# Kernel optimization log

Hardware: AMD Instinct MI355X
Metric: run time of the kernel (lower is better)

## Reference

```python
import jax, jax.numpy as jnp
import numpy as np

N_NODES = 50000
N_EDGES = 800000
IN_FEATS = 64
HIDDEN = 64
NUM_CLASSES = 32


def _graph_conv(x, src, dst, W, b, n_nodes):
    # DGL GraphConv, norm='both', allow_zero_in_degree=True:
    # out = D_in^{-1/2} * (A^T @ (D_out^{-1/2} * x)) @ W + b, degrees clamped to >=1
    e = src.shape[0]
    ones = jnp.ones((e,), dtype=x.dtype)
    out_deg = jax.ops.segment_sum(ones, src, num_segments=n_nodes)
    in_deg = jax.ops.segment_sum(ones, dst, num_segments=n_nodes)
    norm_src = jax.lax.rsqrt(jnp.maximum(out_deg, 1.0))[:, None]
    norm_dst = jax.lax.rsqrt(jnp.maximum(in_deg, 1.0))[:, None]
    h = x * norm_src                                   # [N, d]
    agg = jax.ops.segment_sum(h[src], dst, num_segments=n_nodes)  # gather+scatter over edges
    return (agg * norm_dst) @ W + b


def setup_inputs() -> dict:
    key = jax.random.key(0)
    k1, k2, k3, k4, k5 = jax.random.split(key, 5)
    features = jax.random.normal(k1, (N_NODES, IN_FEATS), dtype=jnp.float32)
    src = jax.random.randint(k2, (N_EDGES,), 0, N_NODES, dtype=jnp.int32)
    dst = jax.random.randint(k3, (N_EDGES,), 0, N_NODES, dtype=jnp.int32)
    W1 = jax.random.normal(k4, (IN_FEATS, HIDDEN), dtype=jnp.float32) * (1.0 / np.sqrt(IN_FEATS))
    b1 = jnp.zeros((HIDDEN,), dtype=jnp.float32)
    W2 = jax.random.normal(k5, (HIDDEN, NUM_CLASSES), dtype=jnp.float32) * (1.0 / np.sqrt(HIDDEN))
    b2 = jnp.zeros((NUM_CLASSES,), dtype=jnp.float32)
    return {"features": features, "src": src, "dst": dst,
            "W1": W1, "b1": b1, "W2": W2, "b2": b2}


def reference(features, src, dst, W1, b1, W2, b2) -> jnp.ndarray:
    n = features.shape[0]
    h = jax.nn.relu(_graph_conv(features, src, dst, W1, b1, n))
    out = _graph_conv(h, src, dst, W2, b2, n)
    # single canonical etype -> mean over one-element stack is identity
    return out
```

## Files before the change

### kernel.cpp

```cpp
#include <hip/hip_runtime.h>
#include <hip/hip_bf16.h>

#define N_NODES 50000
#define N_EDGES 800000
#define F 64
#define C 32
#define CAP 48

#define NPB   800
#define EPB   1000
#define NBUCK 196
#define SEGCAP 5120

#define G1_BLOCKS   2048
#define GOUT_BLOCKS 2048

static __device__ __forceinline__ float bflo(int u) {
    return __uint_as_float(((unsigned)u) << 16);
}
static __device__ __forceinline__ float bfhi(int u) {
    return __uint_as_float(((unsigned)u) & 0xffff0000u);
}
static __device__ __forceinline__ unsigned short f2bf(float f) {
    __hip_bfloat16 h = __float2bfloat16(f);
    return *reinterpret_cast<unsigned short*>(&h);
}

__global__ void part_fused_kernel(const int* __restrict__ src, const int* __restrict__ dst,
                                  int* __restrict__ odeg, int* __restrict__ gseg,
                                  int* __restrict__ edge_d) {
    __shared__ int hd[NBUCK];
    int t = threadIdx.x;
    for (int i = t; i < NBUCK; i += 256) hd[i] = 0;
    __syncthreads();
    int b0 = blockIdx.x * EPB;
    const int4* s4 = reinterpret_cast<const int4*>(src + b0);
    const int4* d4 = reinterpret_cast<const int4*>(dst + b0);
    for (int i = t; i < EPB / 4; i += 256) {
        int4 dv = d4[i];
        int4 sv = s4[i];
        atomicAdd(&hd[dv.x >> 8], 1); atomicAdd(&hd[dv.y >> 8], 1);
        atomicAdd(&hd[dv.z >> 8], 1); atomicAdd(&hd[dv.w >> 8], 1);
        atomicAdd(&odeg[sv.x], 1); atomicAdd(&odeg[sv.y], 1);
        atomicAdd(&odeg[sv.z], 1); atomicAdd(&odeg[sv.w], 1);
    }
    __syncthreads();
    for (int i = t; i < NBUCK; i += 256) {
        int c = hd[i];
        int base = atomicAdd(&gseg[i], c);
        hd[i] = i * SEGCAP + base;
    }
    __syncthreads();
    for (int i = t; i < EPB / 4; i += 256) {
        int4 dv = d4[i];
        int4 sv = s4[i];
        int p;
        p = atomicAdd(&hd[dv.x >> 8], 1); edge_d[p] = ((dv.x & 255) << 16) | sv.x;
        p = atomicAdd(&hd[dv.y >> 8], 1); edge_d[p] = ((dv.y & 255) << 16) | sv.y;
        p = atomicAdd(&hd[dv.z >> 8], 1); edge_d[p] = ((dv.z & 255) << 16) | sv.z;
        p = atomicAdd(&hd[dv.w >> 8], 1); edge_d[p] = ((dv.w & 255) << 16) | sv.w;
    }
}

__global__ void bucket_build_kernel(const int* __restrict__ edge_d,
                                    const int* __restrict__ gseg,
                                    const int* __restrict__ odeg,
                                    unsigned short* __restrict__ csr,
                                    float4* __restrict__ meta) {
    __shared__ int cur[256];
    int t = threadIdx.x;
    int bucket = blockIdx.x;
    cur[t] = 0;
    __syncthreads();
    int len = gseg[bucket];
    if (len > SEGCAP) len = SEGCAP;
    int lo = bucket * SEGCAP, hi = lo + len;
    for (int i = lo + t; i < hi; i += 256) {
        int pd = edge_d[i];
        int dlow = pd >> 16;
        int s = pd & 0xFFFF;
        int pos = atomicAdd(&cur[dlow], 1);
        if (pos < CAP)
            csr[(size_t)(bucket * 256 + dlow) * CAP + pos] = (unsigned short)s;
    }
    __syncthreads();
    int node = bucket * 256 + t;
    if (node < N_NODES) {
        int c = cur[t] < CAP ? cur[t] : CAP;
        float4 m;
        m.x = rsqrtf(fmaxf((float)c, 1.0f));
        m.y = rsqrtf(fmaxf((float)odeg[node], 1.0f));
        m.z = __int_as_float(c);
        m.w = 0.f;
        meta[node] = m;
    }
}

__global__ void gemm_y_kernel(const float* __restrict__ x,
                              const float4* __restrict__ meta,
                              const float* __restrict__ W,
                              __hip_bfloat16* __restrict__ y) {
    __shared__ float sW[F * F];
    __shared__ float srow[16][F];
    int t = threadIdx.x;
    for (int i = t; i < F * F; i += 256) sW[i] = W[i];
    int j = t & 63;
    int w = t >> 6;
    int base = blockIdx.x * 16;
    for (int r = w; r < 16; r += 4) srow[r][j] = x[(size_t)(base + r) * F + j];
    __syncthreads();
    float a0 = 0, a1 = 0, a2 = 0, a3 = 0;
#pragma unroll
    for (int k = 0; k < F; k++) {
        float wv = sW[k * F + j];
        a0 += srow[w * 4 + 0][k] * wv;
        a1 += srow[w * 4 + 1][k] * wv;
        a2 += srow[w * 4 + 2][k] * wv;
        a3 += srow[w * 4 + 3][k] * wv;
    }
    int n0 = base + w * 4;
    y[(size_t)(n0 + 0) * F + j] = __float2bfloat16(a0 * meta[n0 + 0].y);
    y[(size_t)(n0 + 1) * F + j] = __float2bfloat16(a1 * meta[n0 + 1].y);
    y[(size_t)(n0 + 2) * F + j] = __float2bfloat16(a2 * meta[n0 + 2].y);
    y[(size_t)(n0 + 3) * F + j] = __float2bfloat16(a3 * meta[n0 + 3].y);
}

__global__ void gather64_gemv_kernel(const __hip_bfloat16* __restrict__ y,
                                     const unsigned short* __restrict__ csr,
                                     const float4* __restrict__ meta,
                                     const float* __restrict__ b1,
                                     const float* __restrict__ W2,
                                     __hip_bfloat16* __restrict__ gt) {
    __shared__ float sW[F * C];
    int t = threadIdx.x;
    for (int i = t; i < F * C; i += 256) sW[i] = W2[i];
    __syncthreads();
    int w    = t >> 6;
    int lane = t & 63;
    int g  = lane >> 3;
    int fo = (lane & 7) * 8;
    int j    = lane & 31;
    int half = lane >> 5;
    const float4 b1a = *reinterpret_cast<const float4*>(b1 + fo);
    const float4 b1b = *reinterpret_cast<const float4*>(b1 + fo + 4);
    const unsigned short* ytab = reinterpret_cast<const unsigned short*>(y);
    const int STRIDE = G1_BLOCKS * 4;

    int node = blockIdx.x * 4 + w;
    float4 pm = meta[node];
    const unsigned short* prow = csr + (size_t)node * CAP;
    int pr0 = prow[g], pr1 = prow[8 + g], pr2 = prow[16 + g];

    while (node < N_NODES) {
        float nd = pm.x, ns = pm.y;
        int n = __float_as_int(pm.z);
        int r0 = pr0, r1 = pr1, r2 = pr2;
        int nxt = node + STRIDE;
        int pf = (nxt < N_NODES) ? nxt : node;

        int ss0 = (g      < n) ? r0 : 0;  float m0 = (g      < n) ? 1.f : 0.f;
        int ss1 = (8  + g < n) ? r1 : 0;  float m1 = (8  + g < n) ? 1.f : 0.f;
        int ss2 = (16 + g < n) ? r2 : 0;  float m2 = (16 + g < n) ? 1.f : 0.f;

        const int4 v0 = *reinterpret_cast<const int4*>(ytab + (size_t)ss0 * F + fo);
        const int4 v1 = *reinterpret_cast<const int4*>(ytab + (size_t)ss1 * F + fo);
        const int4 v2 = *reinterpret_cast<const int4*>(ytab + (size_t)ss2 * F + fo);

        pm = meta[pf];
        const unsigned short* nrow = csr + (size_t)pf * CAP;
        pr0 = nrow[g]; pr1 = nrow[8 + g]; pr2 = nrow[16 + g];

        float a0, a1, a2, a3, a4, a5, a6, a7;
        a0 = m0 * bflo(v0.x); a1 = m0 * bfhi(v0.x);
        a2 = m0 * bflo(v0.y); a3 = m0 * bfhi(v0.y);
        a4 = m0 * bflo(v0.z); a5 = m0 * bfhi(v0.z);
        a6 = m0 * bflo(v0.w); a7 = m0 * bfhi(v0.w);

#define G1_ACC(vv, mm)                                                        \
        a0 = fmaf(mm, bflo(vv.x), a0); a1 = fmaf(mm, bfhi(vv.x), a1);         \
        a2 = fmaf(mm, bflo(vv.y), a2); a3 = fmaf(mm, bfhi(vv.y), a3);         \
        a4 = fmaf(mm, bflo(vv.z), a4); a5 = fmaf(mm, bfhi(vv.z), a5);         \
        a6 = fmaf(mm, bflo(vv.w), a6); a7 = fmaf(mm, bfhi(vv.w), a7);
        G1_ACC(v1, m1)
        G1_ACC(v2, m2)

        if (__builtin_expect(n > 24, 0)) {
            const unsigned short* row = csr + (size_t)node * CAP;
            int r3 = row[24 + g], r4 = row[32 + g], r5 = row[40 + g];
            int ss3 = (24 + g < n) ? r3 : 0;  float m3 = (24 + g < n) ? 1.f : 0.f;
            int ss4 = (32 + g < n) ? r4 : 0;  float m4 = (32 + g < n) ? 1.f : 0.f;
            int ss5 = (40 + g < n) ? r5 : 0;  float m5 = (40 + g < n) ? 1.f : 0.f;
            const int4 v3 = *reinterpret_cast<const int4*>(ytab + (size_t)ss3 * F + fo);
            const int4 v4 = *reinterpret_cast<const int4*>(ytab + (size_t)ss4 * F + fo);
            const int4 v5 = *reinterpret_cast<const int4*>(ytab + (size_t)ss5 * F + fo);
            G1_ACC(v3, m3)
            G1_ACC(v4, m4)
            G1_ACC(v5, m5)
        }
#undef G1_ACC

#define G1_RED(mk)                                                           \
        a0 += __shfl_xor(a0, mk); a1 += __shfl_xor(a1, mk);                  \
        a2 += __shfl_xor(a2, mk); a3 += __shfl_xor(a3, mk);                  \
        a4 += __shfl_xor(a4, mk); a5 += __shfl_xor(a5, mk);                  \
        a6 += __shfl_xor(a6, mk); a7 += __shfl_xor(a7, mk);
        G1_RED(8)
        G1_RED(16)
        G1_RED(32)
#undef G1_RED

        float hh[8];
        hh[0] = fmaxf(fmaf(a0, nd, b1a.x), 0.f) * ns;
        hh[1] = fmaxf(fmaf(a1, nd, b1a.y), 0.f) * ns;
        hh[2] = fmaxf(fmaf(a2, nd, b1a.z), 0.f) * ns;
        hh[3] = fmaxf(fmaf(a3, nd, b1a.w), 0.f) * ns;
        hh[4] = fmaxf(fmaf(a4, nd, b1b.x), 0.f) * ns;
        hh[5] = fmaxf(fmaf(a5, nd, b1b.y), 0.f) * ns;
        hh[6] = fmaxf(fmaf(a6, nd, b1b.z), 0.f) * ns;
        hh[7] = fmaxf(fmaf(a7, nd, b1b.w), 0.f) * ns;

        float o = 0.f;
#pragma unroll
        for (int k = 0; k < 32; k++) {
            float hv = __shfl(hh[k & 7], (half << 2) + (k >> 3));
            o = fmaf(hv, sW[(half * 32 + k) * C + j], o);
        }
        o += __shfl_down(o, 32);
        if (half == 0)
            __builtin_nontemporal_store(f2bf(o),
                reinterpret_cast<unsigned short*>(gt) + (size_t)node * C + j);
        node = nxt;
    }
}

__global__ void gather_out_kernel(const __hip_bfloat16* __restrict__ gt,
                                  const unsigned short* __restrict__ csr,
                                  const float4* __restrict__ meta,
                                  const float* __restrict__ b2,
                                  float* __restrict__ out) {
    int t = threadIdx.x;
    int w = t >> 6;
    int lane = t & 63;
    int g  = lane >> 3;
    int fo = (lane & 7) * 4;
    const unsigned short* tab = reinterpret_cast<const unsigned short*>(gt);
    const float4 bb = *reinterpret_cast<const float4*>(b2 + fo);
    const int STRIDE = GOUT_BLOCKS * 4;

    int node = blockIdx.x * 4 + w;
    float4 pm = meta[node];
    const unsigned short* prow = csr + (size_t)node * CAP;
    int pr0 = prow[g], pr1 = prow[8 + g], pr2 = prow[16 + g];

    while (node < N_NODES) {
        float nd = pm.x;
        int n = __float_as_int(pm.z);
        int r0 = pr0, r1 = pr1, r2 = pr2;
        int nxt = node + STRIDE;
        int pf = (nxt < N_NODES) ? nxt : node;

        int ss0 = (g      < n) ? r0 : 0;  float m0 = (g      < n) ? 1.f : 0.f;
        int ss1 = (8  + g < n) ? r1 : 0;  float m1 = (8  + g < n) ? 1.f : 0.f;
        int ss2 = (16 + g < n) ? r2 : 0;  float m2 = (16 + g < n) ? 1.f : 0.f;

        const int2 v0 = *reinterpret_cast<const int2*>(tab + (size_t)ss0 * C + fo);
        const int2 v1 = *reinterpret_cast<const int2*>(tab + (size_t)ss1 * C + fo);
        const int2 v2 = *reinterpret_cast<const int2*>(tab + (size_t)ss2 * C + fo);

        pm = meta[pf];
        const unsigned short* nrow = csr + (size_t)pf * CAP;
        pr0 = nrow[g]; pr1 = nrow[8 + g]; pr2 = nrow[16 + g];

        float a0, a1, a2, a3;
        a0 = m0 * bflo(v0.x); a1 = m0 * bfhi(v0.x);
        a2 = m0 * bflo(v0.y); a3 = m0 * bfhi(v0.y);

#define G2_ACC(vv, mm)                                                        \
        a0 = fmaf(mm, bflo(vv.x), a0); a1 = fmaf(mm, bfhi(vv.x), a1);         \
        a2 = fmaf(mm, bflo(vv.y), a2); a3 = fmaf(mm, bfhi(vv.y), a3);
        G2_ACC(v1, m1)
        G2_ACC(v2, m2)

        if (__builtin_expect(n > 24, 0)) {
            const unsigned short* row = csr + (size_t)node * CAP;
            int r3 = row[24 + g], r4 = row[32 + g], r5 = row[40 + g];
            int ss3 = (24 + g < n) ? r3 : 0;  float m3 = (24 + g < n) ? 1.f : 0.f;
            int ss4 = (32 + g < n) ? r4 : 0;  float m4 = (32 + g < n) ? 1.f : 0.f;
            int ss5 = (40 + g < n) ? r5 : 0;  float m5 = (40 + g < n) ? 1.f : 0.f;
            const int2 v3 = *reinterpret_cast<const int2*>(tab + (size_t)ss3 * C + fo);
            const int2 v4 = *reinterpret_cast<const int2*>(tab + (size_t)ss4 * C + fo);
            const int2 v5 = *reinterpret_cast<const int2*>(tab + (size_t)ss5 * C + fo);
            G2_ACC(v3, m3)
            G2_ACC(v4, m4)
            G2_ACC(v5, m5)
        }
#undef G2_ACC

        a0 += __shfl_xor(a0, 8);  a1 += __shfl_xor(a1, 8);
        a2 += __shfl_xor(a2, 8);  a3 += __shfl_xor(a3, 8);
        a0 += __shfl_xor(a0, 16); a1 += __shfl_xor(a1, 16);
        a2 += __shfl_xor(a2, 16); a3 += __shfl_xor(a3, 16);
        a0 += __shfl_xor(a0, 32); a1 += __shfl_xor(a1, 32);
        a2 += __shfl_xor(a2, 32); a3 += __shfl_xor(a3, 32);

        if (lane < 8) {
            float o0 = fmaf(a0, nd, bb.x);
            float o1 = fmaf(a1, nd, bb.y);
            float o2 = fmaf(a2, nd, bb.z);
            float o3 = fmaf(a3, nd, bb.w);
            unsigned long long p0 = ((unsigned long long)__float_as_uint(o0)) |
                                    ((unsigned long long)__float_as_uint(o1) << 32);
            unsigned long long p1 = ((unsigned long long)__float_as_uint(o2)) |
                                    ((unsigned long long)__float_as_uint(o3) << 32);
            unsigned long long* po = reinterpret_cast<unsigned long long*>(
                out + (size_t)node * C + fo);
            __builtin_nontemporal_store(p0, po);
            __builtin_nontemporal_store(p1, po + 1);
        }
        node = nxt;
    }
}

extern "C" void kernel_launch(void* const* d_in, const int* in_sizes, int n_in,
                              void* d_out, int out_size, void* d_ws, size_t ws_size,
                              hipStream_t stream) {
    const float* features = (const float*)d_in[0];
    const int*   src      = (const int*)d_in[1];
    const int*   dst      = (const int*)d_in[2];
    const float* W1       = (const float*)d_in[3];
    const float* b1       = (const float*)d_in[4];
    const float* W2       = (const float*)d_in[5];
    const float* b2       = (const float*)d_in[6];
    float* out = (float*)d_out;

    char* p = (char*)d_ws;
    float4* meta = (float4*)p;            p += (size_t)N_NODES * 16;
    unsigned short* csr = (unsigned short*)p; p += (size_t)N_NODES * CAP * 2;
    __hip_bfloat16* y  = (__hip_bfloat16*)p;  p += (size_t)N_NODES * F * 2;
    __hip_bfloat16* gt = (__hip_bfloat16*)p;

    int* edge_d = (int*)y;
    int* odeg   = (int*)gt;
    int* gseg   = odeg + N_NODES;

    hipMemsetAsync(odeg, 0, (size_t)(N_NODES + 256) * 4, stream);

    part_fused_kernel<<<NPB, 256, 0, stream>>>(src, dst, odeg, gseg, edge_d);
    bucket_build_kernel<<<NBUCK, 256, 0, stream>>>(edge_d, gseg, odeg, csr, meta);

    gemm_y_kernel<<<N_NODES / 16, 256, 0, stream>>>(features, meta, W1, y);
    gather64_gemv_kernel<<<G1_BLOCKS, 256, 0, stream>>>(y, csr, meta, b1, W2, gt);

    gather_out_kernel<<<GOUT_BLOCKS, 256, 0, stream>>>(gt, csr, meta, b2, out);
}
```

Measured before the change: 198.2 us.

## Compute out-degrees via bucketed source partition instead of global atomics

Out-degree counting no longer uses 800k global atomics on an odeg array. Source low bytes are partitioned into per-bucket segments using shared-memory histograms, and each bucket block then counts per-node out-degree in shared memory. This removes the scattered global atomics and shrinks the memset to the segment counters. In exchange it writes and reads an extra byte-per-edge array and adds a second counting pass in the bucket kernel.

```diff
diff --git a/kernel.cpp b/kernel.cpp
--- a/kernel.cpp
+++ b/kernel.cpp
@@ -27,11 +27,11 @@
 }
 
 __global__ void part_fused_kernel(const int* __restrict__ src, const int* __restrict__ dst,
-                                  int* __restrict__ odeg, int* __restrict__ gseg,
-                                  int* __restrict__ edge_d) {
-    __shared__ int hd[NBUCK];
-    int t = threadIdx.x;
-    for (int i = t; i < NBUCK; i += 256) hd[i] = 0;
+                                  int* __restrict__ gseg,
+                                  int* __restrict__ edge_d, unsigned char* __restrict__ edge_s) {
+    __shared__ int hd[NBUCK], hs[NBUCK];
+    int t = threadIdx.x;
+    for (int i = t; i < NBUCK; i += 256) { hd[i] = 0; hs[i] = 0; }
     __syncthreads();
     int b0 = blockIdx.x * EPB;
     const int4* s4 = reinterpret_cast<const int4*>(src + b0);
@@ -41,14 +41,13 @@
         int4 sv = s4[i];
         atomicAdd(&hd[dv.x >> 8], 1); atomicAdd(&hd[dv.y >> 8], 1);
         atomicAdd(&hd[dv.z >> 8], 1); atomicAdd(&hd[dv.w >> 8], 1);
-        atomicAdd(&odeg[sv.x], 1); atomicAdd(&odeg[sv.y], 1);
-        atomicAdd(&odeg[sv.z], 1); atomicAdd(&odeg[sv.w], 1);
+        atomicAdd(&hs[sv.x >> 8], 1); atomicAdd(&hs[sv.y >> 8], 1);
+        atomicAdd(&hs[sv.z >> 8], 1); atomicAdd(&hs[sv.w >> 8], 1);
     }
     __syncthreads();
     for (int i = t; i < NBUCK; i += 256) {
-        int c = hd[i];
-        int base = atomicAdd(&gseg[i], c);
-        hd[i] = i * SEGCAP + base;
+        hd[i] = i * SEGCAP + atomicAdd(&gseg[i], hd[i]);
+        hs[i] = i * SEGCAP + atomicAdd(&gseg[NBUCK + i], hs[i]);
     }
     __syncthreads();
     for (int i = t; i < EPB / 4; i += 256) {
@@ -59,23 +58,29 @@
         p = atomicAdd(&hd[dv.y >> 8], 1); edge_d[p] = ((dv.y & 255) << 16) | sv.y;
         p = atomicAdd(&hd[dv.z >> 8], 1); edge_d[p] = ((dv.z & 255) << 16) | sv.z;
         p = atomicAdd(&hd[dv.w >> 8], 1); edge_d[p] = ((dv.w & 255) << 16) | sv.w;
+        p = atomicAdd(&hs[sv.x >> 8], 1); edge_s[p] = (unsigned char)(sv.x & 255);
+        p = atomicAdd(&hs[sv.y >> 8], 1); edge_s[p] = (unsigned char)(sv.y & 255);
+        p = atomicAdd(&hs[sv.z >> 8], 1); edge_s[p] = (unsigned char)(sv.z & 255);
+        p = atomicAdd(&hs[sv.w >> 8], 1); edge_s[p] = (unsigned char)(sv.w & 255);
     }
 }
 
 __global__ void bucket_build_kernel(const int* __restrict__ edge_d,
+                                    const unsigned char* __restrict__ edge_s,
                                     const int* __restrict__ gseg,
-                                    const int* __restrict__ odeg,
                                     unsigned short* __restrict__ csr,
                                     float4* __restrict__ meta) {
     __shared__ int cur[256];
+    __shared__ int hsm[256];
     int t = threadIdx.x;
     int bucket = blockIdx.x;
     cur[t] = 0;
-    __syncthreads();
-    int len = gseg[bucket];
-    if (len > SEGCAP) len = SEGCAP;
-    int lo = bucket * SEGCAP, hi = lo + len;
-    for (int i = lo + t; i < hi; i += 256) {
+    hsm[t] = 0;
+    __syncthreads();
+    int lend = gseg[bucket];           if (lend > SEGCAP) lend = SEGCAP;
+    int lens = gseg[NBUCK + bucket];   if (lens > SEGCAP) lens = SEGCAP;
+    int lo = bucket * SEGCAP;
+    for (int i = lo + t; i < lo + lend; i += 256) {
         int pd = edge_d[i];
         int dlow = pd >> 16;
         int s = pd & 0xFFFF;
@@ -83,13 +88,16 @@
         if (pos < CAP)
             csr[(size_t)(bucket * 256 + dlow) * CAP + pos] = (unsigned short)s;
     }
+    for (int i = lo + t; i < lo + lens; i += 256) {
+        atomicAdd(&hsm[edge_s[i]], 1);
+    }
     __syncthreads();
     int node = bucket * 256 + t;
     if (node < N_NODES) {
         int c = cur[t] < CAP ? cur[t] : CAP;
         float4 m;
         m.x = rsqrtf(fmaxf((float)c, 1.0f));
-        m.y = rsqrtf(fmaxf((float)odeg[node], 1.0f));
+        m.y = rsqrtf(fmaxf((float)hsm[t], 1.0f));
         m.z = __int_as_float(c);
         m.w = 0.f;
         meta[node] = m;
@@ -340,13 +348,13 @@
     __hip_bfloat16* gt = (__hip_bfloat16*)p;
 
     int* edge_d = (int*)y;
-    int* odeg   = (int*)gt;
-    int* gseg   = odeg + N_NODES;
-
-    hipMemsetAsync(odeg, 0, (size_t)(N_NODES + 256) * 4, stream);
-
-    part_fused_kernel<<<NPB, 256, 0, stream>>>(src, dst, odeg, gseg, edge_d);
-    bucket_build_kernel<<<NBUCK, 256, 0, stream>>>(edge_d, gseg, odeg, csr, meta);
+    unsigned char* edge_s = (unsigned char*)(edge_d + NBUCK * SEGCAP);
+    int* gseg   = (int*)gt;
+
+    hipMemsetAsync(gseg, 0, (size_t)(2 * NBUCK) * 4, stream);
+
+    part_fused_kernel<<<NPB, 256, 0, stream>>>(src, dst, gseg, edge_d, edge_s);
+    bucket_build_kernel<<<NBUCK, 256, 0, stream>>>(edge_d, edge_s, gseg, csr, meta);
 
     gemm_y_kernel<<<N_NODES / 16, 256, 0, stream>>>(features, meta, W1, y);
     gather64_gemv_kernel<<<G1_BLOCKS, 256, 0, stream>>>(y, csr, meta, b1, W2, gt);
```

Result: faster. 189.6 us (-4.3%).
